# Kernel tuning notes

Hardware: AMD Instinct MI355X
Metric: run time of the kernel (lower is better)

Reference implementation:

```python
import jax, jax.numpy as jnp
import numpy as np

H = 1024  # rnn hidden size

def _lstm_layer(x, h0, c0, Wih, Whh, bih, bhh):
    """x: [B,T,F]; returns (ys [B,T,H], hT [B,H], cT [B,H]). Torch gate order i,f,g,o."""
    xs = jnp.swapaxes(x, 0, 1)                       # [T,B,F]
    pre = xs @ Wih.T + (bih + bhh)                   # hoist input GEMM out of scan
    WhhT = Whh.T
    def step(carry, pre_t):
        h, c = carry
        g = pre_t + h @ WhhT                         # [B,4H]
        i, f, gg, o = jnp.split(g, 4, axis=-1)
        c = jax.nn.sigmoid(f) * c + jax.nn.sigmoid(i) * jnp.tanh(gg)
        h = jax.nn.sigmoid(o) * jnp.tanh(c)
        return (h, c), h
    (hT, cT), ys = jax.lax.scan(step, (h0, c0), pre)
    return jnp.swapaxes(ys, 0, 1), hT, cT

def _lstm_stack(x, h0, c0, params):
    """h0,c0: [L,B,H]; params: list of (Wih,Whh,bih,bhh) per layer."""
    hs, cs = [], []
    out = x
    for l, (Wih, Whh, bih, bhh) in enumerate(params):
        out, hT, cT = _lstm_layer(out, h0[l], c0[l], Wih, Whh, bih, bhh)
        hs.append(hT); cs.append(cT)
    return out, jnp.stack(hs), jnp.stack(cs)


def setup_inputs() -> dict:
    key = jax.random.key(0)
    ks = jax.random.split(key, 24)
    B, Tin, F = 128, 256, 8
    Ty = 129
    s = 0.05
    d = {
        'x': jax.random.normal(ks[0], (B, Tin, F), jnp.float32),
        'y': jax.random.normal(ks[1], (B, Ty), jnp.float32),
        # encoder LSTM (2 layers, input 8 -> H)
        'enc_Wih0': s * jax.random.normal(ks[2], (4 * H, F), jnp.float32),
        'enc_Whh0': s * jax.random.normal(ks[3], (4 * H, H), jnp.float32),
        'enc_bih0': s * jax.random.normal(ks[4], (4 * H,), jnp.float32),
        'enc_bhh0': s * jax.random.normal(ks[5], (4 * H,), jnp.float32),
        'enc_Wih1': s * jax.random.normal(ks[6], (4 * H, H), jnp.float32),
        'enc_Whh1': s * jax.random.normal(ks[7], (4 * H, H), jnp.float32),
        'enc_bih1': s * jax.random.normal(ks[8], (4 * H,), jnp.float32),
        'enc_bhh1': s * jax.random.normal(ks[9], (4 * H,), jnp.float32),
        # decoder LSTM (2 layers, input 1 -> H)
        'dec_Wih0': s * jax.random.normal(ks[10], (4 * H, 1), jnp.float32),
        'dec_Whh0': s * jax.random.normal(ks[11], (4 * H, H), jnp.float32),
        'dec_bih0': s * jax.random.normal(ks[12], (4 * H,), jnp.float32),
        'dec_bhh0': s * jax.random.normal(ks[13], (4 * H,), jnp.float32),
        'dec_Wih1': s * jax.random.normal(ks[14], (4 * H, H), jnp.float32),
        'dec_Whh1': s * jax.random.normal(ks[15], (4 * H, H), jnp.float32),
        'dec_bih1': s * jax.random.normal(ks[16], (4 * H,), jnp.float32),
        'dec_bhh1': s * jax.random.normal(ks[17], (4 * H,), jnp.float32),
        # mean / std predictor heads (H -> 1)
        'Wmu': s * jax.random.normal(ks[18], (1, H), jnp.float32),
        'bmu': s * jax.random.normal(ks[19], (1,), jnp.float32),
        'Wsig': s * jax.random.normal(ks[20], (1, H), jnp.float32),
        'bsig': s * jax.random.normal(ks[21], (1,), jnp.float32),
    }
    return d


def reference(x, y,
              enc_Wih0, enc_Whh0, enc_bih0, enc_bhh0,
              enc_Wih1, enc_Whh1, enc_bih1, enc_bhh1,
              dec_Wih0, dec_Whh0, dec_bih0, dec_bhh0,
              dec_Wih1, dec_Whh1, dec_bih1, dec_bhh1,
              Wmu, bmu, Wsig, bsig):
    B = x.shape[0]
    seq_len = y.shape[1] - 1
    L = 2
    h0 = jnp.zeros((L, B, H), x.dtype)
    c0 = jnp.zeros((L, B, H), x.dtype)
    enc_params = [(enc_Wih0, enc_Whh0, enc_bih0, enc_bhh0),
                  (enc_Wih1, enc_Whh1, enc_bih1, enc_bhh1)]
    dec_params = [(dec_Wih0, dec_Whh0, dec_bih0, dec_bhh0),
                  (dec_Wih1, dec_Whh1, dec_bih1, dec_bhh1)]
    _, eh, ec = _lstm_stack(x, h0, c0, enc_params)
    # teacher_forcing = 1.0: decoder inputs are ground-truth y[:, 0:seq_len]
    dec_in = y[:, :seq_len, None]                     # [B,S,1]
    dec_out, _, _ = _lstm_stack(dec_in, eh, ec, dec_params)  # [B,S,H]
    mu = dec_out @ Wmu.T + bmu                        # [B,S,1]
    sigma = jax.nn.softplus(dec_out @ Wsig.T + bsig)  # [B,S,1]
    output_collection = jnp.zeros((B, seq_len, 1), x.dtype)
    return output_collection, mu, sigma
```

## Files before the change

kernel.cpp:

```cpp
#include <hip/hip_runtime.h>
#include <stdint.h>

#define BATCH  128
#define TENC   256
#define TDEC   128
#define NSTEPS 384
#define GP     2176
#define HP     2048
#define HOFF   69632
#define SMEMSZ 135168
#define EXP    65
#define MUSOFF 106496

typedef __attribute__((ext_vector_type(8))) short s16x8;
typedef __attribute__((ext_vector_type(4))) float f32x4;

#define OFF_XBF 0u
#define OFF_YBF 524288u
#define OFF_H0  557056u
#define OFF_H1  1081344u
#define OFF_MU  1605632u
#define OFF_SIG 1671168u
#define OFF_BAR 1736704u
#define WS_END  1738752u

__device__ __forceinline__ unsigned short f2bf(float f) {
  unsigned u = __float_as_uint(f);
  u = u + 0x7fffu + ((u >> 16) & 1u);
  return (unsigned short)(u >> 16);
}
__device__ __forceinline__ float sigm(float x) { return 1.f / (1.f + __expf(-x)); }
__device__ __forceinline__ float tanh_f(float x) {
  float a = fabsf(x);
  float e = __expf(-2.f * a);
  float t = (1.f - e) / (1.f + e);
  return x < 0.f ? -t : t;
}

__device__ __forceinline__ void glds16c(const void* g, void* l) {
  __builtin_amdgcn_global_load_lds((const __attribute__((address_space(1))) void*)g,
                                   (__attribute__((address_space(3))) void*)l, 16, 0, 17);
}
__device__ __forceinline__ unsigned ldcoh(const unsigned* p) {
  unsigned v;
  asm volatile("global_load_dword %0, %1, off sc0 sc1\n\ts_waitcnt vmcnt(0)"
               : "=v"(v) : "v"(p) : "memory");
  return v;
}
__device__ __forceinline__ void stcoh(unsigned* p, unsigned v) {
  asm volatile("global_store_dword %0, %1, off sc0 sc1" :: "v"(p), "v"(v) : "memory");
}
__device__ __forceinline__ void pollcnt(const unsigned* p, unsigned target) {
  for (;;) {
    unsigned v = ldcoh(p);
    if ((int)v >= (int)target) break;
    __builtin_amdgcn_s_sleep(1);
  }
}

#define BARRIER() do { __builtin_amdgcn_s_barrier(); asm volatile("" ::: "memory"); } while (0)
#define WAIT_LGKM() asm volatile("s_waitcnt lgkmcnt(0)" ::: "memory")
#define WAIT_VM()   asm volatile("s_waitcnt vmcnt(0)" ::: "memory")
#define WAIT_BOTH() asm volatile("s_waitcnt vmcnt(0) lgkmcnt(0)" ::: "memory")

__device__ __forceinline__ void load_weights(
    s16x8 (&wfa)[9][4], s16x8 (&wfb)[16][4],
    int w, int u0, int l15, int khi,
    const float* W0h, const float* W0x, int xk,
    const float* W1x, const float* W1h) {
#pragma unroll
  for (int j = 0; j < 9; ++j) {
    int kst = w + 4 * j;
#pragma unroll
    for (int n = 0; n < 4; ++n) {
      int g = n * 1024 + u0 + l15;
      s16x8 v;
#pragma unroll
      for (int e = 0; e < 8; ++e) ((unsigned short*)&v)[e] = 0;
      if (kst < 32) {
        const float* p = W0h + (size_t)g * 1024 + kst * 32 + khi * 8;
#pragma unroll
        for (int e = 0; e < 8; ++e) ((unsigned short*)&v)[e] = f2bf(p[e]);
      } else if (kst == 32) {
        if (khi == 0) {
#pragma unroll
          for (int e = 0; e < 8; ++e)
            if (e < xk) ((unsigned short*)&v)[e] = f2bf(W0x[(size_t)g * xk + e]);
        }
      }
      wfa[j][n] = v;
    }
  }
#pragma unroll
  for (int j = 0; j < 16; ++j) {
    int kst = w + 4 * j;
#pragma unroll
    for (int n = 0; n < 4; ++n) {
      int g = n * 1024 + u0 + l15;
      const float* p = (kst < 32)
          ? (W1x + (size_t)g * 1024 + kst * 32 + khi * 8)
          : (W1h + (size_t)g * 1024 + (kst - 32) * 32 + khi * 8);
      s16x8 v;
#pragma unroll
      for (int e = 0; e < 8; ++e) ((unsigned short*)&v)[e] = f2bf(p[e]);
      wfb[j][n] = v;
    }
  }
}

__global__ void cvt_inputs(const float* __restrict__ x, const float* __restrict__ y,
                           unsigned short* __restrict__ xbf, unsigned short* __restrict__ ybf) {
  int i = blockIdx.x * 256 + threadIdx.x;
  if (i < 262144) xbf[i] = f2bf(x[i]);
  if (i < 16384) {
    int b = i >> 7, t = i & 127;
    ybf[i] = f2bf(y[b * 129 + t]);
  }
}

__global__ void __launch_bounds__(256, 1) lstm_main(
    const float* __restrict__ eWx0, const float* __restrict__ eWh0,
    const float* __restrict__ eB0a, const float* __restrict__ eB0b,
    const float* __restrict__ eWx1, const float* __restrict__ eWh1,
    const float* __restrict__ eB1a, const float* __restrict__ eB1b,
    const float* __restrict__ dWx0, const float* __restrict__ dWh0,
    const float* __restrict__ dB0a, const float* __restrict__ dB0b,
    const float* __restrict__ dWx1, const float* __restrict__ dWh1,
    const float* __restrict__ dB1a, const float* __restrict__ dB1b,
    const float* __restrict__ Wmu, const float* __restrict__ Wsig,
    const unsigned short* __restrict__ xbf, const unsigned short* __restrict__ ybf,
    unsigned short* h0buf, unsigned short* h1buf,
    float* mu_acc, float* sig_acc, unsigned* bars) {
  __shared__ char smem[SMEMSZ];

  const int tid = threadIdx.x;
  const int wg = blockIdx.x;
  const int w = tid >> 6;
  const int lane = tid & 63;
  const int l15 = lane & 15;
  const int khi = lane >> 4;
  const int btile = wg & 3;
  const int utile = wg >> 2;
  const int u0 = utile << 4;
  const int r0 = btile << 5;
  const int key = (l15 & 7) << 4;

  unsigned* cnt1 = bars + btile * 64;
  unsigned* cnt2 = cnt1 + 16;

  const int erow = tid >> 3;
  const int uslot = tid & 7;

  s16x8 wfa[9][4];
  s16x8 wfb[16][4];
  load_weights(wfa, wfb, w, u0, l15, khi, eWh0, eWx0, 8, eWx1, eWh1);

  float b0s[2][4], b1s[2][4];
#pragma unroll
  for (int jj = 0; jj < 2; ++jj) {
    int u = u0 + uslot * 2 + jj;
#pragma unroll
    for (int n = 0; n < 4; ++n) {
      b0s[jj][n] = eB0a[n * 1024 + u] + eB0b[n * 1024 + u];
      b1s[jj][n] = eB1a[n * 1024 + u] + eB1b[n * 1024 + u];
    }
  }
  const float wm0 = Wmu[u0 + uslot * 2], wm1 = Wmu[u0 + uslot * 2 + 1];
  const float wg0 = Wsig[u0 + uslot * 2], wg1 = Wsig[u0 + uslot * 2 + 1];

  float c0a = 0.f, c0b = 0.f, c1a = 0.f, c1b = 0.f;

  {
    s16x8 z;
#pragma unroll
    for (int e = 0; e < 8; ++e) ((unsigned short*)&z)[e] = 0;
    for (int o = tid * 16; o < HOFF; o += 4096) *(s16x8*)(smem + o) = z;
  }
  __syncthreads();

  for (int s = 0; s < NSTEPS; ++s) {
    const int enc = (s < 256) ? 1 : 0;
    const int t = enc ? s : (s - 256);
    const int par = s & 1;

    if (tid < 32) {
      char* wb = smem + tid * GP + 2048;
      s16x8 z;
#pragma unroll
      for (int e = 0; e < 8; ++e) ((unsigned short*)&z)[e] = 0;
#pragma unroll
      for (int q = 0; q < 8; ++q) *(s16x8*)(wb + q * 16) = z;
      int slot = (tid & 7) << 4;
      if (enc) {
        *(s16x8*)(wb + slot) = *(const s16x8*)(xbf + (((size_t)(r0 + tid) * TENC + t) << 3));
      } else {
        s16x8 yv = z;
        ((unsigned short*)&yv)[0] = ybf[(r0 + tid) * TDEC + t];
        *(s16x8*)(wb + slot) = yv;
      }
    }
    if (s == 256) {
      load_weights(wfa, wfb, w, u0, l15, khi, dWh0, dWx0, 1, dWx1, dWh1);
#pragma unroll
      for (int jj = 0; jj < 2; ++jj) {
        int u = u0 + uslot * 2 + jj;
#pragma unroll
        for (int n = 0; n < 4; ++n) {
          b0s[jj][n] = dB0a[n * 1024 + u] + dB0b[n * 1024 + u];
          b1s[jj][n] = dB1a[n * 1024 + u] + dB1b[n * 1024 + u];
        }
      }
    }
    WAIT_LGKM();
    BARRIER();

    f32x4 acc[2][4];
#pragma unroll
    for (int m = 0; m < 2; ++m)
#pragma unroll
      for (int n = 0; n < 4; ++n) acc[m][n] = {0.f, 0.f, 0.f, 0.f};
#pragma unroll
    for (int j = 0; j < 8; ++j) {
      int off = (w + 4 * j) << 6;
#pragma unroll
      for (int m = 0; m < 2; ++m) {
        const s16x8 af = *(const s16x8*)(smem + (m * 16 + l15) * GP + ((off + khi * 16) ^ key));
#pragma unroll
        for (int n = 0; n < 4; ++n)
          acc[m][n] = __builtin_amdgcn_mfma_f32_16x16x32_bf16(af, wfa[j][n], acc[m][n], 0, 0, 0);
      }
    }
    if (w == 0) {
#pragma unroll
      for (int m = 0; m < 2; ++m) {
        const s16x8 af = *(const s16x8*)(smem + (m * 16 + l15) * GP + ((2048 + khi * 16) ^ key));
#pragma unroll
        for (int n = 0; n < 4; ++n)
          acc[m][n] = __builtin_amdgcn_mfma_f32_16x16x32_bf16(af, wfa[8][n], acc[m][n], 0, 0, 0);
      }
    }

    pollcnt(cnt2, 64u * (unsigned)s);
#pragma unroll
    for (int rr = 0; rr < 8; ++rr) {
      int row = w * 8 + rr;
      const char* src = (const char*)(h1buf + (((size_t)par * BATCH + r0 + row) << 10));
      char* dst = smem + HOFF + row * HP;
      glds16c(src + lane * 16, dst);
      glds16c(src + 1024 + lane * 16, dst + 1024);
    }

    WAIT_LGKM();
    BARRIER();
    {
      float* exw = (float*)smem;
#pragma unroll
      for (int m = 0; m < 2; ++m)
#pragma unroll
        for (int n = 0; n < 4; ++n)
#pragma unroll
          for (int r = 0; r < 4; ++r)
            exw[(w * 32 + m * 16 + khi * 4 + r) * EXP + n * 16 + l15] = acc[m][n][r];
    }
    WAIT_LGKM();
    BARRIER();

    {
      const float* exw = (const float*)smem;
      unsigned short* hb = h0buf + (((size_t)(par ^ 1) * BATCH + r0 + erow) << 10);
      float hv[2];
#pragma unroll
      for (int jj = 0; jj < 2; ++jj) {
        int u = uslot * 2 + jj;
        float g[4];
#pragma unroll
        for (int n = 0; n < 4; ++n) {
          int c = n * 16 + u;
          g[n] = exw[erow * EXP + c] + exw[(32 + erow) * EXP + c]
               + exw[(64 + erow) * EXP + c] + exw[(96 + erow) * EXP + c] + b0s[jj][n];
        }
        float cv = jj ? c0b : c0a;
        float cn = sigm(g[1]) * cv + sigm(g[0]) * tanh_f(g[2]);
        if (jj) c0b = cn; else c0a = cn;
        hv[jj] = sigm(g[3]) * tanh_f(cn);
      }
      int uswz = (u0 + uslot * 2) ^ ((erow & 7) << 3);
      unsigned pk = (unsigned)f2bf(hv[0]) | ((unsigned)f2bf(hv[1]) << 16);
      stcoh((unsigned*)(hb + uswz), pk);
    }
    WAIT_VM();
    BARRIER();
    if (tid == 0) atomicAdd(cnt1, 1u);

    f32x4 bcc[2][4];
#pragma unroll
    for (int m = 0; m < 2; ++m)
#pragma unroll
      for (int n = 0; n < 4; ++n) bcc[m][n] = {0.f, 0.f, 0.f, 0.f};
#pragma unroll
    for (int j = 8; j < 12; ++j) {
      int off = (w + 4 * (j - 8)) << 6;
#pragma unroll
      for (int m = 0; m < 2; ++m) {
        const s16x8 af = *(const s16x8*)(smem + HOFF + (m * 16 + l15) * HP + ((off + khi * 16) ^ key));
#pragma unroll
        for (int n = 0; n < 4; ++n)
          bcc[m][n] = __builtin_amdgcn_mfma_f32_16x16x32_bf16(af, wfb[j][n], bcc[m][n], 0, 0, 0);
      }
    }
    pollcnt(cnt1, 64u * (unsigned)(s + 1));
#pragma unroll
    for (int rr = 0; rr < 8; ++rr) {
      int row = w * 8 + rr;
      const char* src = (const char*)(h0buf + (((size_t)(par ^ 1) * BATCH + r0 + row) << 10));
      char* dst = smem + row * GP;
      glds16c(src + lane * 16, dst);
      glds16c(src + 1024 + lane * 16, dst + 1024);
    }
#pragma unroll
    for (int j = 12; j < 16; ++j) {
      int off = (w + 4 * (j - 8)) << 6;
#pragma unroll
      for (int m = 0; m < 2; ++m) {
        const s16x8 af = *(const s16x8*)(smem + HOFF + (m * 16 + l15) * HP + ((off + khi * 16) ^ key));
#pragma unroll
        for (int n = 0; n < 4; ++n)
          bcc[m][n] = __builtin_amdgcn_mfma_f32_16x16x32_bf16(af, wfb[j][n], bcc[m][n], 0, 0, 0);
      }
    }
    WAIT_VM();
    BARRIER();
#pragma unroll
    for (int j = 0; j < 8; ++j) {
      int off = (w + 4 * j) << 6;
#pragma unroll
      for (int m = 0; m < 2; ++m) {
        const s16x8 af = *(const s16x8*)(smem + (m * 16 + l15) * GP + ((off + khi * 16) ^ key));
#pragma unroll
        for (int n = 0; n < 4; ++n)
          bcc[m][n] = __builtin_amdgcn_mfma_f32_16x16x32_bf16(af, wfb[j][n], bcc[m][n], 0, 0, 0);
      }
    }
    WAIT_LGKM();
    BARRIER();
    {
      float* exw = (float*)(smem + HOFF);
#pragma unroll
      for (int m = 0; m < 2; ++m)
#pragma unroll
        for (int n = 0; n < 4; ++n)
#pragma unroll
          for (int r = 0; r < 4; ++r)
            exw[(w * 32 + m * 16 + khi * 4 + r) * EXP + n * 16 + l15] = bcc[m][n][r];
    }
    WAIT_LGKM();
    BARRIER();
    {
      const float* exw = (const float*)(smem + HOFF);
      unsigned short* hb = h1buf + (((size_t)(par ^ 1) * BATCH + r0 + erow) << 10);
      float hv[2];
#pragma unroll
      for (int jj = 0; jj < 2; ++jj) {
        int u = uslot * 2 + jj;
        float g[4];
#pragma unroll
        for (int n = 0; n < 4; ++n) {
          int c = n * 16 + u;
          g[n] = exw[erow * EXP + c] + exw[(32 + erow) * EXP + c]
               + exw[(64 + erow) * EXP + c] + exw[(96 + erow) * EXP + c] + b1s[jj][n];
        }
        float cv = jj ? c1b : c1a;
        float cn = sigm(g[1]) * cv + sigm(g[0]) * tanh_f(g[2]);
        if (jj) c1b = cn; else c1a = cn;
        hv[jj] = sigm(g[3]) * tanh_f(cn);
      }
      int uswz = (u0 + uslot * 2) ^ ((erow & 7) << 3);
      unsigned pk = (unsigned)f2bf(hv[0]) | ((unsigned)f2bf(hv[1]) << 16);
      stcoh((unsigned*)(hb + uswz), pk);
      if (!enc) {
        float* muS = (float*)(smem + MUSOFF);
        muS[uslot * 64 + erow] = hv[0] * wm0 + hv[1] * wm1;
        muS[uslot * 64 + 32 + erow] = hv[0] * wg0 + hv[1] * wg1;
      }
    }
    WAIT_BOTH();
    BARRIER();
    if (tid == 0) atomicAdd(cnt2, 1u);
    if (!enc && tid < 64) {
      const float* muS = (const float*)(smem + MUSOFF);
      float sum = 0.f;
#pragma unroll
      for (int q = 0; q < 8; ++q) sum += muS[q * 64 + tid];
      if (tid < 32) atomicAdd(mu_acc + t * BATCH + r0 + tid, sum);
      else          atomicAdd(sig_acc + t * BATCH + r0 + (tid - 32), sum);
    }
  }
}

__global__ void finalize_k(const float* __restrict__ mu_acc, const float* __restrict__ sig_acc,
                           const float* __restrict__ bmu, const float* __restrict__ bsig,
                           float* __restrict__ out) {
  int i = blockIdx.x * 256 + threadIdx.x;
  if (i >= 16384) return;
  int b = i >> 7, t = i & 127;
  float m = mu_acc[t * 128 + b] + bmu[0];
  float sv = sig_acc[t * 128 + b] + bsig[0];
  float sp = sv > 20.f ? sv : log1pf(__expf(sv));
  out[16384 + i] = m;
  out[32768 + i] = sp;
}

extern "C" void kernel_launch(void* const* d_in, const int* in_sizes, int n_in,
                              void* d_out, int out_size, void* d_ws, size_t ws_size,
                              hipStream_t stream) {
  const float* x    = (const float*)d_in[0];
  const float* y    = (const float*)d_in[1];
  const float* eWx0 = (const float*)d_in[2];
  const float* eWh0 = (const float*)d_in[3];
  const float* eB0a = (const float*)d_in[4];
  const float* eB0b = (const float*)d_in[5];
  const float* eWx1 = (const float*)d_in[6];
  const float* eWh1 = (const float*)d_in[7];
  const float* eB1a = (const float*)d_in[8];
  const float* eB1b = (const float*)d_in[9];
  const float* dWx0 = (const float*)d_in[10];
  const float* dWh0 = (const float*)d_in[11];
  const float* dB0a = (const float*)d_in[12];
  const float* dB0b = (const float*)d_in[13];
  const float* dWx1 = (const float*)d_in[14];
  const float* dWh1 = (const float*)d_in[15];
  const float* dB1a = (const float*)d_in[16];
  const float* dB1b = (const float*)d_in[17];
  const float* Wmu  = (const float*)d_in[18];
  const float* bmu  = (const float*)d_in[19];
  const float* Wsig = (const float*)d_in[20];
  const float* bsig = (const float*)d_in[21];

  char* ws = (char*)d_ws;
  unsigned short* xbf = (unsigned short*)(ws + OFF_XBF);
  unsigned short* ybf = (unsigned short*)(ws + OFF_YBF);
  unsigned short* h0b = (unsigned short*)(ws + OFF_H0);
  unsigned short* h1b = (unsigned short*)(ws + OFF_H1);
  float* mu_acc  = (float*)(ws + OFF_MU);
  float* sig_acc = (float*)(ws + OFF_SIG);
  unsigned* bars = (unsigned*)(ws + OFF_BAR);

  hipMemsetAsync(ws + OFF_H0, 0, WS_END - OFF_H0, stream);
  hipMemsetAsync(d_out, 0, (size_t)16384 * 4, stream);

  cvt_inputs<<<1024, 256, 0, stream>>>(x, y, xbf, ybf);
  lstm_main<<<256, 256, 0, stream>>>(eWx0, eWh0, eB0a, eB0b, eWx1, eWh1, eB1a, eB1b,
                                     dWx0, dWh0, dB0a, dB0b, dWx1, dWh1, dB1a, dB1b,
                                     Wmu, Wsig, xbf, ybf, h0b, h1b, mu_acc, sig_acc, bars);
  finalize_k<<<64, 256, 0, stream>>>(mu_acc, sig_acc, bmu, bsig, (float*)d_out);
}
```

Baseline: 3.946 ms.

## Wavefront-skew the two LSTM layers so layer1 step k-1 overlaps layer0 step k

Restructures the persistent recurrent loop into a skewed schedule. Each iteration k computes layer-0 step k and layer-1 step k-1. Both consume the same h0 state loaded once into LDS, and separate exchange buffers let the two gate reductions coexist. This cuts the number of cross-workgroup poll/barrier round trips per timestep and lets layer-1's recurrent GEMM overlap the h0 global load. The cost is an extra iteration, more LDS, and a subtler handoff of parity and counters, including the decoder weight swap being split across k=256 and k=257.

```diff
diff --git a/kernel.cpp b/kernel.cpp
--- a/kernel.cpp
+++ b/kernel.cpp
@@ -8,9 +8,11 @@
 #define GP     2176
 #define HP     2048
 #define HOFF   69632
-#define SMEMSZ 135168
+#define EX0OFF HOFF
+#define EX1OFF (HOFF + 33280)
+#define MUSOFF (HOFF + 66560)
+#define SMEMSZ (HOFF + 68608)
 #define EXP    65
-#define MUSOFF 106496
 
 typedef __attribute__((ext_vector_type(8))) short s16x8;
 typedef __attribute__((ext_vector_type(4))) float f32x4;
@@ -63,11 +65,9 @@
 #define WAIT_VM()   asm volatile("s_waitcnt vmcnt(0)" ::: "memory")
 #define WAIT_BOTH() asm volatile("s_waitcnt vmcnt(0) lgkmcnt(0)" ::: "memory")
 
-__device__ __forceinline__ void load_weights(
-    s16x8 (&wfa)[9][4], s16x8 (&wfb)[16][4],
-    int w, int u0, int l15, int khi,
-    const float* W0h, const float* W0x, int xk,
-    const float* W1x, const float* W1h) {
+__device__ __forceinline__ void load_wa(
+    s16x8 (&wfa)[9][4], int w, int u0, int l15, int khi,
+    const float* W0h, const float* W0x, int xk) {
 #pragma unroll
   for (int j = 0; j < 9; ++j) {
     int kst = w + 4 * j;
@@ -91,6 +91,10 @@
       wfa[j][n] = v;
     }
   }
+}
+__device__ __forceinline__ void load_wb(
+    s16x8 (&wfb)[16][4], int w, int u0, int l15, int khi,
+    const float* W1x, const float* W1h) {
 #pragma unroll
   for (int j = 0; j < 16; ++j) {
     int kst = w + 4 * j;
@@ -153,7 +157,8 @@
 
   s16x8 wfa[9][4];
   s16x8 wfb[16][4];
-  load_weights(wfa, wfb, w, u0, l15, khi, eWh0, eWx0, 8, eWx1, eWh1);
+  load_wa(wfa, w, u0, l15, khi, eWh0, eWx0, 8);
+  load_wb(wfb, w, u0, l15, khi, eWx1, eWh1);
 
   float b0s[2][4], b1s[2][4];
 #pragma unroll
@@ -174,100 +179,122 @@
     s16x8 z;
 #pragma unroll
     for (int e = 0; e < 8; ++e) ((unsigned short*)&z)[e] = 0;
-    for (int o = tid * 16; o < HOFF; o += 4096) *(s16x8*)(smem + o) = z;
+    for (int o = tid * 16; o < SMEMSZ; o += 4096) *(s16x8*)(smem + o) = z;
   }
   __syncthreads();
 
-  for (int s = 0; s < NSTEPS; ++s) {
-    const int enc = (s < 256) ? 1 : 0;
-    const int t = enc ? s : (s - 256);
-    const int par = s & 1;
-
-    if (tid < 32) {
-      char* wb = smem + tid * GP + 2048;
-      s16x8 z;
-#pragma unroll
-      for (int e = 0; e < 8; ++e) ((unsigned short*)&z)[e] = 0;
-#pragma unroll
-      for (int q = 0; q < 8; ++q) *(s16x8*)(wb + q * 16) = z;
-      int slot = (tid & 7) << 4;
-      if (enc) {
-        *(s16x8*)(wb + slot) = *(const s16x8*)(xbf + (((size_t)(r0 + tid) * TENC + t) << 3));
+  for (int k = 0; k <= NSTEPS; ++k) {
+    const int doL0 = (k < NSTEPS);
+    const int doL1 = (k > 0);
+    const int par0 = k & 1;
+    const int gpar = par0 ^ 1;
+    const int hpar = (k - 1) & 1;
+
+    if (k > 0) pollcnt(cnt1, 64u * (unsigned)k);
+    BARRIER();
+
+#pragma unroll
+    for (int rr = 0; rr < 8; ++rr) {
+      int row = w * 8 + rr;
+      const char* src = (const char*)(h0buf + (((size_t)gpar * BATCH + r0 + row) << 10));
+      char* dst = smem + row * GP;
+      glds16c(src + lane * 16, dst);
+      glds16c(src + 1024 + lane * 16, dst + 1024);
+    }
+    if (doL0 && tid < 32) {
+      char* wb = smem + tid * GP + 2048 + ((tid & 7) << 4);
+      int t0 = (k < 256) ? k : (k - 256);
+      if (k < 256) {
+        *(s16x8*)wb = *(const s16x8*)(xbf + (((size_t)(r0 + tid) * TENC + t0) << 3));
       } else {
-        s16x8 yv = z;
-        ((unsigned short*)&yv)[0] = ybf[(r0 + tid) * TDEC + t];
-        *(s16x8*)(wb + slot) = yv;
-      }
-    }
-    if (s == 256) {
-      load_weights(wfa, wfb, w, u0, l15, khi, dWh0, dWx0, 1, dWx1, dWh1);
+        s16x8 yv;
+#pragma unroll
+        for (int e = 0; e < 8; ++e) ((unsigned short*)&yv)[e] = 0;
+        ((unsigned short*)&yv)[0] = ybf[(r0 + tid) * TDEC + t0];
+        *(s16x8*)wb = yv;
+      }
+    }
+    if (k == 256) {
+      load_wa(wfa, w, u0, l15, khi, dWh0, dWx0, 1);
 #pragma unroll
       for (int jj = 0; jj < 2; ++jj) {
         int u = u0 + uslot * 2 + jj;
 #pragma unroll
-        for (int n = 0; n < 4; ++n) {
-          b0s[jj][n] = dB0a[n * 1024 + u] + dB0b[n * 1024 + u];
-          b1s[jj][n] = dB1a[n * 1024 + u] + dB1b[n * 1024 + u];
-        }
-      }
+        for (int n = 0; n < 4; ++n) b0s[jj][n] = dB0a[n * 1024 + u] + dB0b[n * 1024 + u];
+      }
+    }
+    if (k == 257) {
+      load_wb(wfb, w, u0, l15, khi, dWx1, dWh1);
+#pragma unroll
+      for (int jj = 0; jj < 2; ++jj) {
+        int u = u0 + uslot * 2 + jj;
+#pragma unroll
+        for (int n = 0; n < 4; ++n) b1s[jj][n] = dB1a[n * 1024 + u] + dB1b[n * 1024 + u];
+      }
+    }
+
+    f32x4 acc1[2][4];
+#pragma unroll
+    for (int m = 0; m < 2; ++m)
+#pragma unroll
+      for (int n = 0; n < 4; ++n) acc1[m][n] = {0.f, 0.f, 0.f, 0.f};
+    if (doL1) {
+#pragma unroll
+      for (int j = 8; j < 16; ++j) {
+        int off = (w + 4 * (j - 8)) << 6;
+#pragma unroll
+        for (int m = 0; m < 2; ++m) {
+          const s16x8 af = *(const s16x8*)(smem + HOFF + (m * 16 + l15) * HP + ((off + khi * 16) ^ key));
+#pragma unroll
+          for (int n = 0; n < 4; ++n)
+            acc1[m][n] = __builtin_amdgcn_mfma_f32_16x16x32_bf16(af, wfb[j][n], acc1[m][n], 0, 0, 0);
+        }
+      }
+    }
+    WAIT_VM();
+    BARRIER();
+
+    f32x4 acc0[2][4];
+#pragma unroll
+    for (int m = 0; m < 2; ++m)
+#pragma unroll
+      for (int n = 0; n < 4; ++n) acc0[m][n] = {0.f, 0.f, 0.f, 0.f};
+    if (doL0) {
+#pragma unroll
+      for (int j = 0; j < 8; ++j) {
+        int off = (w + 4 * j) << 6;
+#pragma unroll
+        for (int m = 0; m < 2; ++m) {
+          const s16x8 af = *(const s16x8*)(smem + (m * 16 + l15) * GP + ((off + khi * 16) ^ key));
+#pragma unroll
+          for (int n = 0; n < 4; ++n)
+            acc0[m][n] = __builtin_amdgcn_mfma_f32_16x16x32_bf16(af, wfa[j][n], acc0[m][n], 0, 0, 0);
+        }
+      }
+      if (w == 0) {
+#pragma unroll
+        for (int m = 0; m < 2; ++m) {
+          const s16x8 af = *(const s16x8*)(smem + (m * 16 + l15) * GP + ((2048 + khi * 16) ^ key));
+#pragma unroll
+          for (int n = 0; n < 4; ++n)
+            acc0[m][n] = __builtin_amdgcn_mfma_f32_16x16x32_bf16(af, wfa[8][n], acc0[m][n], 0, 0, 0);
+        }
+      }
+      float* exw = (float*)(smem + EX0OFF);
+#pragma unroll
+      for (int m = 0; m < 2; ++m)
+#pragma unroll
+        for (int n = 0; n < 4; ++n)
+#pragma unroll
+          for (int r = 0; r < 4; ++r)
+            exw[(w * 32 + m * 16 + khi * 4 + r) * EXP + n * 16 + l15] = acc0[m][n][r];
     }
     WAIT_LGKM();
     BARRIER();
 
-    f32x4 acc[2][4];
-#pragma unroll
-    for (int m = 0; m < 2; ++m)
-#pragma unroll
-      for (int n = 0; n < 4; ++n) acc[m][n] = {0.f, 0.f, 0.f, 0.f};
-#pragma unroll
-    for (int j = 0; j < 8; ++j) {
-      int off = (w + 4 * j) << 6;
-#pragma unroll
-      for (int m = 0; m < 2; ++m) {
-        const s16x8 af = *(const s16x8*)(smem + (m * 16 + l15) * GP + ((off + khi * 16) ^ key));
-#pragma unroll
-        for (int n = 0; n < 4; ++n)
-          acc[m][n] = __builtin_amdgcn_mfma_f32_16x16x32_bf16(af, wfa[j][n], acc[m][n], 0, 0, 0);
-      }
-    }
-    if (w == 0) {
-#pragma unroll
-      for (int m = 0; m < 2; ++m) {
-        const s16x8 af = *(const s16x8*)(smem + (m * 16 + l15) * GP + ((2048 + khi * 16) ^ key));
-#pragma unroll
-        for (int n = 0; n < 4; ++n)
-          acc[m][n] = __builtin_amdgcn_mfma_f32_16x16x32_bf16(af, wfa[8][n], acc[m][n], 0, 0, 0);
-      }
-    }
-
-    pollcnt(cnt2, 64u * (unsigned)s);
-#pragma unroll
-    for (int rr = 0; rr < 8; ++rr) {
-      int row = w * 8 + rr;
-      const char* src = (const char*)(h1buf + (((size_t)par * BATCH + r0 + row) << 10));
-      char* dst = smem + HOFF + row * HP;
-      glds16c(src + lane * 16, dst);
-      glds16c(src + 1024 + lane * 16, dst + 1024);
-    }
-
-    WAIT_LGKM();
-    BARRIER();
-    {
-      float* exw = (float*)smem;
-#pragma unroll
-      for (int m = 0; m < 2; ++m)
-#pragma unroll
-        for (int n = 0; n < 4; ++n)
-#pragma unroll
-          for (int r = 0; r < 4; ++r)
-            exw[(w * 32 + m * 16 + khi * 4 + r) * EXP + n * 16 + l15] = acc[m][n][r];
-    }
-    WAIT_LGKM();
-    BARRIER();
-
-    {
-      const float* exw = (const float*)smem;
-      unsigned short* hb = h0buf + (((size_t)(par ^ 1) * BATCH + r0 + erow) << 10);
+    if (doL0) {
+      const float* exw = (const float*)(smem + EX0OFF);
+      unsigned short* hb = h0buf + (((size_t)par0 * BATCH + r0 + erow) << 10);
       float hv[2];
 #pragma unroll
       for (int jj = 0; jj < 2; ++jj) {
@@ -290,74 +317,35 @@
     }
     WAIT_VM();
     BARRIER();
-    if (tid == 0) atomicAdd(cnt1, 1u);
-
-    f32x4 bcc[2][4];
-#pragma unroll
-    for (int m = 0; m < 2; ++m)
-#pragma unroll
-      for (int n = 0; n < 4; ++n) bcc[m][n] = {0.f, 0.f, 0.f, 0.f};
-#pragma unroll
-    for (int j = 8; j < 12; ++j) {
-      int off = (w + 4 * (j - 8)) << 6;
-#pragma unroll
-      for (int m = 0; m < 2; ++m) {
-        const s16x8 af = *(const s16x8*)(smem + HOFF + (m * 16 + l15) * HP + ((off + khi * 16) ^ key));
+    if (doL0 && tid == 0) atomicAdd(cnt1, 1u);
+
+    if (doL1) {
+#pragma unroll
+      for (int j = 0; j < 8; ++j) {
+        int off = (w + 4 * j) << 6;
+#pragma unroll
+        for (int m = 0; m < 2; ++m) {
+          const s16x8 af = *(const s16x8*)(smem + (m * 16 + l15) * GP + ((off + khi * 16) ^ key));
+#pragma unroll
+          for (int n = 0; n < 4; ++n)
+            acc1[m][n] = __builtin_amdgcn_mfma_f32_16x16x32_bf16(af, wfb[j][n], acc1[m][n], 0, 0, 0);
+        }
+      }
+      float* exw = (float*)(smem + EX1OFF);
+#pragma unroll
+      for (int m = 0; m < 2; ++m)
 #pragma unroll
         for (int n = 0; n < 4; ++n)
-          bcc[m][n] = __builtin_amdgcn_mfma_f32_16x16x32_bf16(af, wfb[j][n], bcc[m][n], 0, 0, 0);
-      }
-    }
-    pollcnt(cnt1, 64u * (unsigned)(s + 1));
-#pragma unroll
-    for (int rr = 0; rr < 8; ++rr) {
-      int row = w * 8 + rr;
-      const char* src = (const char*)(h0buf + (((size_t)(par ^ 1) * BATCH + r0 + row) << 10));
-      char* dst = smem + row * GP;
-      glds16c(src + lane * 16, dst);
-      glds16c(src + 1024 + lane * 16, dst + 1024);
-    }
-#pragma unroll
-    for (int j = 12; j < 16; ++j) {
-      int off = (w + 4 * (j - 8)) << 6;
-#pragma unroll
-      for (int m = 0; m < 2; ++m) {
-        const s16x8 af = *(const s16x8*)(smem + HOFF + (m * 16 + l15) * HP + ((off + khi * 16) ^ key));
-#pragma unroll
-        for (int n = 0; n < 4; ++n)
-          bcc[m][n] = __builtin_amdgcn_mfma_f32_16x16x32_bf16(af, wfb[j][n], bcc[m][n], 0, 0, 0);
-      }
-    }
-    WAIT_VM();
-    BARRIER();
-#pragma unroll
-    for (int j = 0; j < 8; ++j) {
-      int off = (w + 4 * j) << 6;
-#pragma unroll
-      for (int m = 0; m < 2; ++m) {
-        const s16x8 af = *(const s16x8*)(smem + (m * 16 + l15) * GP + ((off + khi * 16) ^ key));
-#pragma unroll
-        for (int n = 0; n < 4; ++n)
-          bcc[m][n] = __builtin_amdgcn_mfma_f32_16x16x32_bf16(af, wfb[j][n], bcc[m][n], 0, 0, 0);
-      }
+#pragma unroll
+          for (int r = 0; r < 4; ++r)
+            exw[(w * 32 + m * 16 + khi * 4 + r) * EXP + n * 16 + l15] = acc1[m][n][r];
     }
     WAIT_LGKM();
     BARRIER();
-    {
-      float* exw = (float*)(smem + HOFF);
-#pragma unroll
-      for (int m = 0; m < 2; ++m)
-#pragma unroll
-        for (int n = 0; n < 4; ++n)
-#pragma unroll
-          for (int r = 0; r < 4; ++r)
-            exw[(w * 32 + m * 16 + khi * 4 + r) * EXP + n * 16 + l15] = bcc[m][n][r];
-    }
-    WAIT_LGKM();
-    BARRIER();
-    {
-      const float* exw = (const float*)(smem + HOFF);
-      unsigned short* hb = h1buf + (((size_t)(par ^ 1) * BATCH + r0 + erow) << 10);
+
+    if (doL1) {
+      const float* exw = (const float*)(smem + EX1OFF);
+      unsigned short* hb = h1buf + (((size_t)hpar * BATCH + r0 + erow) << 10);
       float hv[2];
 #pragma unroll
       for (int jj = 0; jj < 2; ++jj) {
@@ -377,7 +365,7 @@
       int uswz = (u0 + uslot * 2) ^ ((erow & 7) << 3);
       unsigned pk = (unsigned)f2bf(hv[0]) | ((unsigned)f2bf(hv[1]) << 16);
       stcoh((unsigned*)(hb + uswz), pk);
-      if (!enc) {
+      if (k >= 257) {
         float* muS = (float*)(smem + MUSOFF);
         muS[uslot * 64 + erow] = hv[0] * wm0 + hv[1] * wm1;
         muS[uslot * 64 + 32 + erow] = hv[0] * wg0 + hv[1] * wg1;
@@ -385,14 +373,28 @@
     }
     WAIT_BOTH();
     BARRIER();
-    if (tid == 0) atomicAdd(cnt2, 1u);
-    if (!enc && tid < 64) {
+    if (doL1 && tid == 0) atomicAdd(cnt2, 1u);
+
+    if (k >= 257 && tid < 64) {
       const float* muS = (const float*)(smem + MUSOFF);
       float sum = 0.f;
 #pragma unroll
       for (int q = 0; q < 8; ++q) sum += muS[q * 64 + tid];
-      if (tid < 32) atomicAdd(mu_acc + t * BATCH + r0 + tid, sum);
-      else          atomicAdd(sig_acc + t * BATCH + r0 + (tid - 32), sum);
+      int t1 = k - 257;
+      if (tid < 32) atomicAdd(mu_acc + t1 * BATCH + r0 + tid, sum);
+      else          atomicAdd(sig_acc + t1 * BATCH + r0 + (tid - 32), sum);
+    }
+
+    if (k < NSTEPS) {
+      pollcnt(cnt2, 64u * (unsigned)k);
+#pragma unroll
+      for (int rr = 0; rr < 8; ++rr) {
+        int row = w * 8 + rr;
+        const char* src = (const char*)(h1buf + (((size_t)hpar * BATCH + r0 + row) << 10));
+        char* dst = smem + HOFF + row * HP;
+        glds16c(src + lane * 16, dst);
+        glds16c(src + 1024 + lane * 16, dst + 1024);
+      }
     }
   }
 }
```

Result: slower. 8.916 ms (+126.0%).
